# Optimization experiments

Measured on AMD Instinct MI355X. Metric: run time of the kernel, lower is better.

## Reference

```python
import jax, jax.numpy as jnp
import numpy as np

NB_KERNEL = 16
NUM_POS_EMB = 16
DMAX = 20.0


def _grbf_encode(d):
    # d: (..., ) distances; centers 0..DMAX in NB_KERNEL steps (matches torch.arange(0, 20*(1+1/15), 20/15))
    centers = jnp.linspace(0.0, DMAX, NB_KERNEL, dtype=jnp.float32)
    return jnp.exp(-jnp.square(d[..., None] - centers))


def _positional_embeddings(d):
    # d: (..., ) float offsets
    freq = jnp.exp(jnp.arange(0, NUM_POS_EMB, 2, dtype=jnp.float32) * (-(np.log(10000.0) / NUM_POS_EMB)))
    angles = d[..., None] * freq  # (..., NUM_POS_EMB//2)
    return jnp.concatenate([jnp.cos(angles), jnp.sin(angles)], axis=-1)


def setup_inputs() -> dict:
    key = jax.random.key(0)
    # coordinates in Angstrom-ish scale so pairwise distances span the RBF range
    crd = jax.random.normal(key, (4096, 4, 3), dtype=jnp.float32) * 10.0
    return {"crd": crd, "max_neigh": 64}


def reference(crd, max_neigh):
    nb_var = crd.shape[0]
    nb_neigh = min(max_neigh, nb_var - 1)

    # virtual Cbeta atom from backbone geometry
    b = crd[:, 1] - crd[:, 0]
    c = crd[:, 2] - crd[:, 1]
    a = jnp.cross(b, c)
    Cb = -0.58273431 * a + 0.56802827 * b - 0.54067466 * c + crd[:, 1]
    crd5 = jnp.concatenate([crd, Cb[:, None, :]], axis=1)  # (N, 5, 3)

    # pairwise CA distances, diagonal forced to -1 so self sorts first
    ca = crd5[:, 1]  # (N, 3)
    D = jnp.linalg.norm(ca[:, None, :] - ca[None, :, :], axis=-1)  # (N, N)
    diag = jnp.arange(nb_var)
    D = D.at[diag, diag].set(-1.0)

    # nb_neigh smallest distances (= top_k of -D); self is column 0
    neg_d, idx_pairs = jax.lax.top_k(-D, nb_neigh)  # (N, K)
    d = -neg_d
    d = d.at[:, 0].set(0.0)
    d = jnp.nan_to_num(d, nan=0.0)

    # all-pairs atom distances between residue i (5 atoms) and each neighbor j (5 atoms)
    neigh = crd5[idx_pairs]  # (N, K, 5, 3)
    diff = crd5[:, None, :, None, :] - neigh[:, :, None, :, :]  # (N, K, 5, 5, 3); [i,k,a,b]=crd[i,a]-crd[j,b]
    dist = jnp.linalg.norm(diff, axis=-1).reshape(nb_var, nb_neigh, 25)
    dist = _grbf_encode(dist).reshape(nb_var, nb_neigh, 25 * NB_KERNEL)
    dist = jnp.nan_to_num(dist, nan=0.0)

    # sinusoidal encoding of sequence-index offsets
    offsets = jnp.abs(diag[:, None] - idx_pairs).astype(jnp.float32)  # (N, K)
    pos = _positional_embeddings(offsets)  # (N, K, NUM_POS_EMB)

    return (d, dist, pos, idx_pairs)
```

## Files before the change

kernel.cpp:

```cpp
#include <hip/hip_runtime.h>
#include <math.h>

#define NBV 4096
#define KNE 64
#define D_OFF    0
#define DIST_OFF (NBV*KNE)
#define POS_OFF  (DIST_OFF + NBV*KNE*400)
#define IDX_OFF  (POS_OFF + NBV*KNE*16)

#define WS_CRD5 0
#define WS_CA4  (NBV*16)
#define WS_FLOATS (NBV*16 + NBV*4)

typedef float f4v __attribute__((ext_vector_type(4)));

__device__ __forceinline__ unsigned int f2sort(float f) {
  unsigned int u = __float_as_uint(f);
  return (u & 0x80000000u) ? ~u : (u | 0x80000000u);
}
__device__ __forceinline__ float sort2f(unsigned int s) {
  unsigned int u = (s & 0x80000000u) ? (s & 0x7FFFFFFFu) : ~s;
  return __uint_as_float(u);
}

__device__ __forceinline__ float4 crd5_f4(const float* __restrict__ crd, int r,
                                          int q) {
  if (q < 3) return ((const float4*)crd)[r * 3 + q];
  const float4 a = ((const float4*)crd)[r * 3 + 0];
  const float4 b = ((const float4*)crd)[r * 3 + 1];
  const float4 c = ((const float4*)crd)[r * 3 + 2];
  const float bx = a.w - a.x, by = b.x - a.y, bz = b.y - a.z;
  const float cx = b.z - a.w, cy = b.w - b.x, cz = c.x - b.y;
  const float axv = by * cz - bz * cy;
  const float ayv = bz * cx - bx * cz;
  const float azv = bx * cy - by * cx;
  return make_float4(
      -0.58273431f * axv + 0.56802827f * bx - 0.54067466f * cx + a.w,
      -0.58273431f * ayv + 0.56802827f * by - 0.54067466f * cy + b.x,
      -0.58273431f * azv + 0.56802827f * bz - 0.54067466f * cz + b.y, 0.0f);
}

__global__ __launch_bounds__(256) void prep_k(const float* __restrict__ crd,
                                              float* __restrict__ ws) {
  const int r = blockIdx.x * 256 + threadIdx.x;
  const float4 a = ((const float4*)crd)[r * 3 + 0];
  const float4 b = ((const float4*)crd)[r * 3 + 1];
  const float4 c = ((const float4*)crd)[r * 3 + 2];
  const float bx = a.w - a.x, by = b.x - a.y, bz = b.y - a.z;
  const float cx = b.z - a.w, cy = b.w - b.x, cz = c.x - b.y;
  const float axv = by * cz - bz * cy;
  const float ayv = bz * cx - bx * cz;
  const float azv = bx * cy - by * cx;
  const float cbx = -0.58273431f * axv + 0.56802827f * bx - 0.54067466f * cx + a.w;
  const float cby = -0.58273431f * ayv + 0.56802827f * by - 0.54067466f * cy + b.x;
  const float cbz = -0.58273431f * azv + 0.56802827f * bz - 0.54067466f * cz + b.y;

  float4* row = (float4*)(ws + WS_CRD5 + r * 16);
  row[0] = a;
  row[1] = b;
  row[2] = c;
  row[3] = make_float4(cbx, cby, cbz, 0.0f);
  ((float4*)(ws + WS_CA4))[r] = make_float4(a.w, b.x, b.y, 0.0f);
}

template <bool USE_WS>
__global__ __launch_bounds__(256) void fused_k(const float* __restrict__ crd,
                                               const float* __restrict__ ws,
                                               float* __restrict__ out) {
  const int i = blockIdx.x;
  const int t = threadIdx.x;

  __shared__ float region0[2688];
  __shared__ unsigned long long cand[512];
  __shared__ int jidx[64];
  __shared__ unsigned int cnt;
  __shared__ int selbin;
  __shared__ unsigned int wsum[4];

  unsigned int* hist = (unsigned int*)region0;
  float* rows = region0;
  float* dvals = region0 + 1040;

  for (int b = t; b < 2048; b += 256) hist[b] = 0u;
  if (t == 0) cnt = 0u;
  __syncthreads();

  float cax, cay, caz;
  if (USE_WS) {
    const float4 c4 = ((const float4*)(ws + WS_CA4))[i];
    cax = c4.x; cay = c4.y; caz = c4.z;
  } else {
    cax = crd[i * 12 + 3]; cay = crd[i * 12 + 4]; caz = crd[i * 12 + 5];
  }

  float dv[16];
#pragma unroll
  for (int s = 0; s < 16; s++) {
    const int j = t + 256 * s;
    float jx, jy, jz;
    if (USE_WS) {
      const float4 c4 = ((const float4*)(ws + WS_CA4))[j];
      jx = c4.x; jy = c4.y; jz = c4.z;
    } else {
      jx = crd[j * 12 + 3]; jy = crd[j * 12 + 4]; jz = crd[j * 12 + 5];
    }
    const float dx = cax - jx, dy = cay - jy, dz = caz - jz;
    float f = sqrtf(dx * dx + dy * dy + dz * dz);
    if (j == i) f = -1.0f;
    dv[s] = f;
    int b = (int)(f * 16.0f);
    b = b < 0 ? 0 : (b > 2047 ? 2047 : b);
    atomicAdd(&hist[b], 1u);
  }
  __syncthreads();

  unsigned int bc[8];
  unsigned int loc = 0;
#pragma unroll
  for (int r = 0; r < 8; r++) { bc[r] = hist[t * 8 + r]; loc += bc[r]; }
  const int lane = t & 63, wid = t >> 6;
  unsigned int x = loc;
#pragma unroll
  for (int off = 1; off < 64; off <<= 1) {
    unsigned int y = __shfl_up(x, off, 64);
    if (lane >= off) x += y;
  }
  if (lane == 63) wsum[wid] = x;
  __syncthreads();
  unsigned int woff = 0;
#pragma unroll
  for (int w = 0; w < 4; w++)
    if (w < wid) woff += wsum[w];
  unsigned int c = woff + x - loc;
#pragma unroll
  for (int r = 0; r < 8; r++) {
    if (c < 64u && c + bc[r] >= 64u) selbin = t * 8 + r;
    c += bc[r];
  }
  __syncthreads();
  const int B = selbin;

  const unsigned long long lmask = (1ull << lane) - 1ull;
#pragma unroll
  for (int s = 0; s < 16; s++) {
    const float f = dv[s];
    int b = (int)(f * 16.0f);
    b = b < 0 ? 0 : (b > 2047 ? 2047 : b);
    const bool pred = (b <= B);
    const unsigned long long mask = __ballot(pred);
    unsigned int base = 0;
    if (lane == 0 && mask)
      base = atomicAdd(&cnt, (unsigned int)__popcll(mask));
    base = __shfl(base, 0, 64);
    if (pred) {
      const unsigned int p = base + (unsigned int)__popcll(mask & lmask);
      if (p < 512u) {
        const int j = t + 256 * s;
        cand[p] = (((unsigned long long)f2sort(f)) << 32) | (unsigned int)j;
      }
    }
  }
  __syncthreads();

  {
    unsigned int M = cnt;
    if (M > 512u) M = 512u;
    for (int p = t; p < (int)M; p += 256) {
      const unsigned long long key = cand[p];
      int r = 0;
      for (int q = 0; q < (int)M; q++) r += (cand[q] < key);
      if (r < KNE) {
        const int j = (int)(unsigned int)(key & 0xFFFFFFFFull);
        const float f = sort2f((unsigned int)(key >> 32));
        jidx[r] = j;
        out[D_OFF + i * KNE + r] = (r == 0) ? 0.0f : f;
        out[IDX_OFF + i * KNE + r] = (float)j;
      }
    }
  }
  __syncthreads();

  const int sr = t >> 2, qq = t & 3;
  float4 v, v2;
  if (USE_WS) v = ((const float4*)ws)[jidx[sr] * 4 + qq];
  else        v = crd5_f4(crd, jidx[sr], qq);
  if (t < 4) {
    if (USE_WS) v2 = ((const float4*)ws)[i * 4 + t];
    else        v2 = crd5_f4(crd, i, t);
  }

  {
    const int n = sr, g = qq;
    const int j = jidx[n];
    int di = i - j;
    if (di < 0) di = -di;
    const float offv = (float)di;
    const bool hi = (g & 1);
    const float fA = hi ? 0.01f                   : 1.0f;
    const float fB = hi ? 0.0031622776601683794f  : 0.31622776601683794f;
    const float fC = hi ? 0.001f                  : 0.1f;
    const float fD = hi ? 0.00031622776601683794f : 0.031622776601683791f;
    float s0, c0, s1, c1, s2, c2, s3, c3;
    sincosf(offv * fA, &s0, &c0);
    sincosf(offv * fB, &s1, &c1);
    sincosf(offv * fC, &s2, &c2);
    sincosf(offv * fD, &s3, &c3);
    f4v o;
    if (g < 2) o = (f4v){c0, c1, c2, c3};
    else       o = (f4v){s0, s1, s2, s3};
    f4v* pv = (f4v*)(out + POS_OFF) + (size_t)(i * KNE + n) * 4 + g;
    __builtin_nontemporal_store(o, pv);
  }

  ((float4*)rows)[sr * 4 + qq] = v;
  if (t < 4) ((float4*)rows)[64 * 4 + t] = v2;
  __syncthreads();

#pragma unroll
  for (int it = 0; it < 7; it++) {
    const int pid = t + 256 * it;
    if (pid < 1600) {
      const int k = pid / 25;
      const int p = pid - k * 25;
      const int p0 = p / 5;
      const int p1 = p - p0 * 5;
      const float dx = rows[64 * 16 + p0 * 3 + 0] - rows[k * 16 + p1 * 3 + 0];
      const float dy = rows[64 * 16 + p0 * 3 + 1] - rows[k * 16 + p1 * 3 + 1];
      const float dz = rows[64 * 16 + p0 * 3 + 2] - rows[k * 16 + p1 * 3 + 2];
      dvals[pid] = sqrtf(dx * dx + dy * dy + dz * dz);
    }
  }
  __syncthreads();

  const float step = 20.0f / 15.0f;
  const float TWO_S = 2.6666667f;
  const float S2 = 1.7777778f;
  const float RHO = 0.02856550f;
  f4v* dst = (f4v*)(out + DIST_OFF) + (size_t)i * 6400;
#pragma unroll
  for (int s = 0; s < 25; s++) {
    const int f4i = t + 256 * s;
    const int pair = f4i >> 2;
    const float cb0 = (float)((f4i & 3) * 4) * step;
    float u = dvals[pair] - cb0;
    u = fminf(u, 16.0f);
    float e = __expf(-u * u);
    float q = __expf(fmaf(TWO_S, u, -S2));
    f4v o;
    o.x = e;
    e *= q;           o.y = e;
    q *= RHO; e *= q; o.z = e;
    q *= RHO; e *= q; o.w = e;
    __builtin_nontemporal_store(o, dst + f4i);
  }
}

extern "C" void kernel_launch(void* const* d_in, const int* in_sizes, int n_in,
                              void* d_out, int out_size, void* d_ws, size_t ws_size,
                              hipStream_t stream) {
  const float* crd = (const float*)d_in[0];
  float* out = (float*)d_out;
  if (ws_size >= (size_t)WS_FLOATS * sizeof(float)) {
    float* ws = (float*)d_ws;
    hipLaunchKernelGGL(prep_k, dim3(NBV / 256), dim3(256), 0, stream, crd, ws);
    hipLaunchKernelGGL(fused_k<true>, dim3(NBV), dim3(256), 0, stream, crd, ws,
                       out);
  } else {
    hipLaunchKernelGGL(fused_k<false>, dim3(NBV), dim3(256), 0, stream, crd,
                       (const float*)nullptr, out);
  }
}
```

Measured before the change: 445.4 us.

## Assign one wavefront per residue with wave-local top-k selection

Replaces the block-per-residue kernel with one where each 64-lane wavefront handles a whole residue, four residues per block. The histogram, bin selection, candidate compaction, rank sort and output writes use wave barriers and per-wave shared memory instead of block-wide __syncthreads and shared atomics on a counter. The histogram is padded to 33 columns to avoid LDS bank conflicts, and distances are recomputed in a second pass rather than held in registers. The cost is less parallelism per residue, a serial per-wave rank sort, and roughly 44KB of LDS per block, which may limit occupancy.

```diff
diff --git a/kernel.cpp b/kernel.cpp
--- a/kernel.cpp
+++ b/kernel.cpp
@@ -63,9 +63,163 @@
   ((float4*)(ws + WS_CA4))[r] = make_float4(a.w, b.x, b.y, 0.0f);
 }
 
-template <bool USE_WS>
+__global__ __launch_bounds__(256) void fused_w(const float* __restrict__ ws,
+                                               float* __restrict__ out) {
+  const int t = threadIdx.x;
+  const int wv = t >> 6;
+  const int lane = t & 63;
+  const int i = blockIdx.x * 4 + wv;
+
+  __shared__ unsigned int histS[4][64 * 33];
+  __shared__ unsigned long long candS[4][512];
+  __shared__ int jidxS[4][64];
+  __shared__ int selBS[4];
+
+  unsigned int* hist = histS[wv];
+  unsigned long long* cand = candS[wv];
+  int* jidx = jidxS[wv];
+  float* rows = (float*)histS[wv];
+
+#pragma unroll
+  for (int idx = lane; idx < 64 * 33; idx += 64) hist[idx] = 0u;
+  __builtin_amdgcn_wave_barrier();
+
+  const float4 ci = ((const float4*)(ws + WS_CA4))[i];
+
+#pragma unroll 4
+  for (int s = 0; s < 64; s++) {
+    const int j = lane + 64 * s;
+    const float4 cj = ((const float4*)(ws + WS_CA4))[j];
+    const float dx = ci.x - cj.x, dy = ci.y - cj.y, dz = ci.z - cj.z;
+    float f = sqrtf(dx * dx + dy * dy + dz * dz);
+    if (j == i) f = -1.0f;
+    int b = (int)(f * 16.0f);
+    b = b < 0 ? 0 : (b > 2047 ? 2047 : b);
+    atomicAdd(&hist[(b >> 5) * 33 + (b & 31)], 1u);
+  }
+  __builtin_amdgcn_wave_barrier();
+
+  unsigned int lsum = 0;
+#pragma unroll
+  for (int r = 0; r < 32; r++) lsum += hist[lane * 33 + r];
+  unsigned int x = lsum;
+#pragma unroll
+  for (int off = 1; off < 64; off <<= 1) {
+    unsigned int y = __shfl_up(x, off, 64);
+    if (lane >= off) x += y;
+  }
+  const unsigned int cumB = x - lsum;
+  const unsigned long long bal = __ballot(cumB + lsum >= 64u);
+  const int L = __ffsll(bal) - 1;
+  if (lane == L) {
+    unsigned int c = cumB;
+    int B = 32 * L + 31;
+    for (int r = 0; r < 32; r++) {
+      c += hist[L * 33 + r];
+      if (c >= 64u) { B = 32 * L + r; break; }
+    }
+    selBS[wv] = B;
+  }
+  __builtin_amdgcn_wave_barrier();
+  const int B = selBS[wv];
+
+  unsigned int base = 0;
+  const unsigned long long lmask = (1ull << lane) - 1ull;
+#pragma unroll 4
+  for (int s = 0; s < 64; s++) {
+    const int j = lane + 64 * s;
+    const float4 cj = ((const float4*)(ws + WS_CA4))[j];
+    const float dx = ci.x - cj.x, dy = ci.y - cj.y, dz = ci.z - cj.z;
+    float f = sqrtf(dx * dx + dy * dy + dz * dz);
+    if (j == i) f = -1.0f;
+    int b = (int)(f * 16.0f);
+    b = b < 0 ? 0 : (b > 2047 ? 2047 : b);
+    const bool pred = (b <= B);
+    const unsigned long long mask = __ballot(pred);
+    if (pred) {
+      const unsigned int p = base + (unsigned int)__popcll(mask & lmask);
+      if (p < 512u)
+        cand[p] = (((unsigned long long)f2sort(f)) << 32) | (unsigned int)j;
+    }
+    base += (unsigned int)__popcll(mask);
+  }
+  __builtin_amdgcn_wave_barrier();
+  unsigned int M = base;
+  if (M > 512u) M = 512u;
+
+  for (unsigned int p = lane; p < M; p += 64) {
+    const unsigned long long key = cand[p];
+    int r = 0;
+    for (unsigned int q = 0; q < M; q++) r += (cand[q] < key);
+    if (r < KNE) {
+      const int j = (int)(unsigned int)(key & 0xFFFFFFFFull);
+      const float f = sort2f((unsigned int)(key >> 32));
+      jidx[r] = j;
+      out[D_OFF + (size_t)i * KNE + r] = (r == 0) ? 0.0f : f;
+      out[IDX_OFF + (size_t)i * KNE + r] = (float)j;
+    }
+  }
+  __builtin_amdgcn_wave_barrier();
+
+  {
+    const int j = jidx[lane];
+    int di = i - j;
+    if (di < 0) di = -di;
+    const float offv = (float)di;
+    float s0, c0, s1, c1, s2, c2, s3, c3, s4, c4, s5, c5, s6, c6, s7, c7;
+    sincosf(offv * 1.0f, &s0, &c0);
+    sincosf(offv * 0.31622776601683794f, &s1, &c1);
+    sincosf(offv * 0.1f, &s2, &c2);
+    sincosf(offv * 0.031622776601683791f, &s3, &c3);
+    sincosf(offv * 0.01f, &s4, &c4);
+    sincosf(offv * 0.0031622776601683794f, &s5, &c5);
+    sincosf(offv * 0.001f, &s6, &c6);
+    sincosf(offv * 0.00031622776601683794f, &s7, &c7);
+    f4v* pv = (f4v*)(out + POS_OFF) + ((size_t)i * KNE + lane) * 4;
+    __builtin_nontemporal_store((f4v){c0, c1, c2, c3}, pv + 0);
+    __builtin_nontemporal_store((f4v){c4, c5, c6, c7}, pv + 1);
+    __builtin_nontemporal_store((f4v){s0, s1, s2, s3}, pv + 2);
+    __builtin_nontemporal_store((f4v){s4, s5, s6, s7}, pv + 3);
+  }
+
+  for (int idx = lane; idx < 260; idx += 64) {
+    const int row = idx >> 2, q = idx & 3;
+    const int src = (row < 64) ? jidx[row] : i;
+    ((float4*)rows)[idx] = ((const float4*)ws)[src * 4 + q];
+  }
+  __builtin_amdgcn_wave_barrier();
+
+  const float step = 20.0f / 15.0f;
+  const float TWO_S = 2.6666667f;
+  const float S2 = 1.7777778f;
+  const float RHO = 0.02856550f;
+  const float cb0 = (float)((lane & 3) * 4) * step;
+  int k = 0, p = lane >> 2;
+  f4v* dst = (f4v*)(out + DIST_OFF) + (size_t)i * 6400;
+#pragma unroll 4
+  for (int s = 0; s < 100; s++) {
+    const int p0 = (p * 205) >> 10;
+    const int p1 = p - 5 * p0;
+    const float dx = rows[64 * 16 + p0 * 3 + 0] - rows[k * 16 + p1 * 3 + 0];
+    const float dy = rows[64 * 16 + p0 * 3 + 1] - rows[k * 16 + p1 * 3 + 1];
+    const float dz = rows[64 * 16 + p0 * 3 + 2] - rows[k * 16 + p1 * 3 + 2];
+    const float f = sqrtf(dx * dx + dy * dy + dz * dz);
+    float u = f - cb0;
+    u = fminf(u, 16.0f);
+    float e = __expf(-u * u);
+    float q = __expf(fmaf(TWO_S, u, -S2));
+    f4v o;
+    o.x = e;
+    e *= q;           o.y = e;
+    q *= RHO; e *= q; o.z = e;
+    q *= RHO; e *= q; o.w = e;
+    __builtin_nontemporal_store(o, dst + lane + 64 * s);
+    p += 16;
+    if (p >= 25) { p -= 25; k += 1; }
+  }
+}
+
 __global__ __launch_bounds__(256) void fused_k(const float* __restrict__ crd,
-                                               const float* __restrict__ ws,
                                                float* __restrict__ out) {
   const int i = blockIdx.x;
   const int t = threadIdx.x;
@@ -85,26 +239,15 @@
   if (t == 0) cnt = 0u;
   __syncthreads();
 
-  float cax, cay, caz;
-  if (USE_WS) {
-    const float4 c4 = ((const float4*)(ws + WS_CA4))[i];
-    cax = c4.x; cay = c4.y; caz = c4.z;
-  } else {
-    cax = crd[i * 12 + 3]; cay = crd[i * 12 + 4]; caz = crd[i * 12 + 5];
-  }
+  const float cax = crd[i * 12 + 3], cay = crd[i * 12 + 4],
+              caz = crd[i * 12 + 5];
 
   float dv[16];
 #pragma unroll
   for (int s = 0; s < 16; s++) {
     const int j = t + 256 * s;
-    float jx, jy, jz;
-    if (USE_WS) {
-      const float4 c4 = ((const float4*)(ws + WS_CA4))[j];
-      jx = c4.x; jy = c4.y; jz = c4.z;
-    } else {
-      jx = crd[j * 12 + 3]; jy = crd[j * 12 + 4]; jz = crd[j * 12 + 5];
-    }
-    const float dx = cax - jx, dy = cay - jy, dz = caz - jz;
+    const float dx = cax - crd[j * 12 + 3], dy = cay - crd[j * 12 + 4],
+                dz = caz - crd[j * 12 + 5];
     float f = sqrtf(dx * dx + dy * dy + dz * dz);
     if (j == i) f = -1.0f;
     dv[s] = f;
@@ -153,10 +296,10 @@
       base = atomicAdd(&cnt, (unsigned int)__popcll(mask));
     base = __shfl(base, 0, 64);
     if (pred) {
-      const unsigned int p = base + (unsigned int)__popcll(mask & lmask);
-      if (p < 512u) {
+      const unsigned int pp = base + (unsigned int)__popcll(mask & lmask);
+      if (pp < 512u) {
         const int j = t + 256 * s;
-        cand[p] = (((unsigned long long)f2sort(f)) << 32) | (unsigned int)j;
+        cand[pp] = (((unsigned long long)f2sort(f)) << 32) | (unsigned int)j;
       }
     }
   }
@@ -165,8 +308,8 @@
   {
     unsigned int M = cnt;
     if (M > 512u) M = 512u;
-    for (int p = t; p < (int)M; p += 256) {
-      const unsigned long long key = cand[p];
+    for (int pi = t; pi < (int)M; pi += 256) {
+      const unsigned long long key = cand[pi];
       int r = 0;
       for (int q = 0; q < (int)M; q++) r += (cand[q] < key);
       if (r < KNE) {
@@ -182,12 +325,8 @@
 
   const int sr = t >> 2, qq = t & 3;
   float4 v, v2;
-  if (USE_WS) v = ((const float4*)ws)[jidx[sr] * 4 + qq];
-  else        v = crd5_f4(crd, jidx[sr], qq);
-  if (t < 4) {
-    if (USE_WS) v2 = ((const float4*)ws)[i * 4 + t];
-    else        v2 = crd5_f4(crd, i, t);
-  }
+  v = crd5_f4(crd, jidx[sr], qq);
+  if (t < 4) v2 = crd5_f4(crd, i, t);
 
   {
     const int n = sr, g = qq;
@@ -263,10 +402,8 @@
   if (ws_size >= (size_t)WS_FLOATS * sizeof(float)) {
     float* ws = (float*)d_ws;
     hipLaunchKernelGGL(prep_k, dim3(NBV / 256), dim3(256), 0, stream, crd, ws);
-    hipLaunchKernelGGL(fused_k<true>, dim3(NBV), dim3(256), 0, stream, crd, ws,
-                       out);
+    hipLaunchKernelGGL(fused_w, dim3(NBV / 4), dim3(256), 0, stream, ws, out);
   } else {
-    hipLaunchKernelGGL(fused_k<false>, dim3(NBV), dim3(256), 0, stream, crd,
-                       (const float*)nullptr, out);
-  }
-}
+    hipLaunchKernelGGL(fused_k, dim3(NBV), dim3(256), 0, stream, crd, out);
+  }
+}
```

Result: slower. 497.8 us (+11.8%).
